# Performance work log

Hardware: AMD Instinct MI355X
Metric: run time of the kernel (lower is better)

The kernel has to match this reference:

```python
import math
import jax, jax.numpy as jnp
import numpy as np

STEP = 0.1
EPS = 1e-12


def _laplacian(src, dst, n):
    # dense symmetric-normalized Laplacian from COO edge list (symmetrized, 0/1 weights)
    A = jnp.zeros((n, n), dtype=jnp.float32).at[src, dst].set(1.0)
    A = jnp.maximum(A, A.T)
    deg = A.sum(axis=1)
    dinv = jnp.where(deg > 0, 1.0 / jnp.sqrt(jnp.maximum(deg, 1e-12)), 0.0)
    return jnp.eye(n, dtype=jnp.float32) - dinv[:, None] * A * dinv[None, :]


def _filter_bank(L, bs):
    # rational band-pass bank centered at b in arange(0,2.1,STEP):
    # D_b = sqrt(2)*a * inv((L - b I)^4 + a I),  a = (STEP/2)^4
    n = L.shape[0]
    a = (STEP / 2.0) ** 4
    I = jnp.eye(n, dtype=L.dtype)

    def one(b):
        M1 = L - b * I
        P2 = M1 @ M1
        P4 = P2 @ P2
        return math.sqrt(2.0) * a * jnp.linalg.inv(P4 + a * I)

    return jax.vmap(one)(bs)  # [F, n, n]


def _cdist_mean(e):
    # mean pairwise euclidean distance, safe sqrt on the zero diagonal
    d2 = jnp.sum((e[:, None, :] - e[None, :, :]) ** 2, axis=-1)
    d = jnp.sqrt(jnp.where(d2 > 0, d2, 1.0))
    return jnp.where(d2 > 0, d, 0.0).mean()


def setup_inputs() -> dict:
    key = jax.random.key(0)
    k1, k2, k3, k4, k5 = jax.random.split(key, 5)
    B, N, F0, R, E = 64, 128, 32, 1118, 512
    return {
        "x": jax.random.normal(k1, (B, N, F0), dtype=jnp.float32),
        "random_signal": jax.random.normal(k2, (B, N, R), dtype=jnp.float32),
        "C": jax.random.normal(k3, (21, 1), dtype=jnp.float32),
        "edge_src": jax.random.randint(k4, (B, E), 0, N),
        "edge_dst": jax.random.randint(k5, (B, E), 0, N),
        "num_classes": 4,
    }


def reference(x, random_signal, C, edge_src, edge_dst, num_classes):
    B, N, _ = x.shape
    R = random_signal.shape[-1]
    # torch.normal(0, sqrt(1/R)) random signal concatenated to features
    feats = jnp.concatenate([x, random_signal * math.sqrt(1.0 / R)], axis=-1)  # [B,N,F0+R]
    bs = jnp.arange(0.0, 2.1, STEP, dtype=jnp.float32)  # [21]
    Cn = C / jnp.maximum(jnp.linalg.norm(C, axis=0, keepdims=True), EPS)  # F.normalize(C, dim=0)

    def per_graph(src, dst, xg):
        L = _laplacian(src, dst, N)
        D = _filter_bank(L, bs)                      # [F,N,N]
        L_hat = jnp.einsum('fnm,f->nm', D, Cn[:, 0])  # D.permute(1,2,0) @ C, squeezed
        A_hat = jnp.eye(N, dtype=xg.dtype) - L_hat
        y = A_hat @ xg                                # [N, F0+R]
        z = y / jnp.maximum(jnp.linalg.norm(y, axis=1, keepdims=True), EPS)
        logits = z @ z.T                              # decode_all on normalized x
        sp = -jnp.abs(logits).sum() / (N * N)         # -||logits||_1 / n^2
        return y.mean(axis=0), sp

    emb, sp_terms = jax.vmap(per_graph)(edge_src, edge_dst, feats)  # [B,D], [B]

    # faithful repeated in-loop division: s_{i+1} = (s_i + t_i)/B  =>  sum_i t_i * B^{-(B-i)}
    i = jnp.arange(B, dtype=jnp.float32)
    w = jnp.exp(-(B - i) * jnp.log(float(B)))
    sparsity_fwd = jnp.sum(sp_terms * w)

    # labels y = arange(B) % num_classes; one positive group (class members) and
    # one negative group (non-members) per class
    idx = np.arange(B)
    hl1 = jnp.float32(0.0)
    hl2 = jnp.float32(0.0)
    for c in range(num_classes):
        pos = jnp.asarray(idx[idx % num_classes == c])
        neg = jnp.asarray(idx[idx % num_classes != c])
        beta = 1.0 / num_classes + 1e-13  # one group per class
        hl1 = hl1 + (-_cdist_mean(emb[neg])) / beta
        hl2 = hl2 + _cdist_mean(emb[pos])

    Fk = C.shape[0]
    dims = jnp.sqrt(jnp.float32(Fk))
    c_l1 = jnp.sum(jnp.abs(C), axis=0)
    c_l2 = jnp.maximum(jnp.linalg.norm(C, axis=0), EPS)
    sparsity_c = jnp.mean((dims - c_l1 / c_l2) / (dims - 1.0))

    return sparsity_c + hl2 + hl1 + sparsity_fwd
```

## Files before the change

### kernel.cpp

```cpp
#include <hip/hip_runtime.h>
#include <math.h>

#define NN 128
#define SM 129
#define TS 132
#define RS 132
#define SS 17
#define SD 130
#define EP 132

typedef double d4 __attribute__((ext_vector_type(4)));

__global__ __launch_bounds__(512, 1) void k1_lap_pow2(
    const int* __restrict__ src, const int* __restrict__ dst,
    int E, float* __restrict__ Lout, double* __restrict__ L2) {
  extern __shared__ float smf[];
  float* dinv = smf + NN * SM;
  const int g   = blockIdx.x;
  const int tid = threadIdx.x;
  const int wv = tid >> 6, ln = tid & 63;
  const int m  = ln & 15, kq = ln >> 4;

  int rIdx[4], cIdx[4];
  {
    d4 z = {0.0, 0.0, 0.0, 0.0};
    d4 pr = __builtin_amdgcn_mfma_f64_16x16x4f64((double)m, 1.0, z, 0, 0, 0);
    d4 pc = __builtin_amdgcn_mfma_f64_16x16x4f64(1.0, (double)m, z, 0, 0, 0);
#pragma unroll
    for (int r = 0; r < 4; ++r) {
      rIdx[r] = ((int)(pr[r] * 0.25 + 0.5)) & 15;
      cIdx[r] = ((int)(pc[r] * 0.25 + 0.5)) & 15;
    }
  }

  for (int e = tid; e < NN * NN; e += 512) {
    int i = e >> 7, j = e & 127;
    smf[i * SM + j] = 0.f;
  }
  __syncthreads();
  const int* s = src + (size_t)g * E;
  const int* d = dst + (size_t)g * E;
  for (int e = tid; e < E; e += 512) {
    int a = s[e], b = d[e];
    smf[a * SM + b] = 1.f;
    smf[b * SM + a] = 1.f;
  }
  __syncthreads();
  if (tid < NN) {
    float acc = 0.f;
    for (int j = 0; j < NN; ++j) acc += smf[tid * SM + j];
    dinv[tid] = (acc > 0.f) ? (float)(1.0 / sqrt((double)acc)) : 0.f;
  }
  __syncthreads();
  float* Lg = Lout + (size_t)g * NN * NN;
  for (int e = tid; e < NN * NN; e += 512) {
    int i = e >> 7, j = e & 127;
    float v = ((i == j) ? 1.f : 0.f) - dinv[i] * dinv[j] * smf[i * SM + j];
    Lg[e] = v;
    smf[i * SM + j] = v;
  }
  __syncthreads();

  d4 acc[8];
#pragma unroll
  for (int cb = 0; cb < 8; ++cb) {
    acc[cb][0] = 0.0; acc[cb][1] = 0.0; acc[cb][2] = 0.0; acc[cb][3] = 0.0;
  }
  for (int kc = 0; kc < 32; ++kc) {
    double a = (double)smf[(16 * wv + m) * SM + 4 * kc + kq];
#pragma unroll
    for (int cb = 0; cb < 8; ++cb) {
      double b = (double)smf[(4 * kc + kq) * SM + 16 * cb + m];
      acc[cb] = __builtin_amdgcn_mfma_f64_16x16x4f64(a, b, acc[cb], 0, 0, 0);
    }
  }
  double* out = L2 + (size_t)g * NN * NN;
#pragma unroll
  for (int cb = 0; cb < 8; ++cb)
#pragma unroll
    for (int r = 0; r < 4; ++r)
      out[(16 * wv + rIdx[r]) * NN + 16 * cb + cIdx[r]] = acc[cb][r];
}

__global__ __launch_bounds__(512, 1) void k1_pow34(
    const float* __restrict__ L, const double* __restrict__ L2,
    double* __restrict__ L3, double* __restrict__ L4) {
  extern __shared__ double Bs[];
  const int bid = blockIdx.x;
  const int g = bid >> 1, job = bid & 1;
  const int tid = threadIdx.x;
  const int wv = tid >> 6, ln = tid & 63;
  const int m  = ln & 15, kq = ln >> 4;

  int rIdx[4], cIdx[4];
  {
    d4 z = {0.0, 0.0, 0.0, 0.0};
    d4 pr = __builtin_amdgcn_mfma_f64_16x16x4f64((double)m, 1.0, z, 0, 0, 0);
    d4 pc = __builtin_amdgcn_mfma_f64_16x16x4f64(1.0, (double)m, z, 0, 0, 0);
#pragma unroll
    for (int r = 0; r < 4; ++r) {
      rIdx[r] = ((int)(pr[r] * 0.25 + 0.5)) & 15;
      cIdx[r] = ((int)(pc[r] * 0.25 + 0.5)) & 15;
    }
  }

  const float*  Lg  = L  + (size_t)g * NN * NN;
  const double* L2g = L2 + (size_t)g * NN * NN;
  if (job == 0) {
    for (int e = tid; e < NN * NN; e += 512) {
      int i = e >> 7, j = e & 127;
      Bs[i * SD + j] = (double)Lg[e];
    }
  } else {
    for (int e = tid; e < NN * NN; e += 512) {
      int i = e >> 7, j = e & 127;
      Bs[i * SD + j] = L2g[e];
    }
  }
  __syncthreads();

  d4 acc[8];
#pragma unroll
  for (int cb = 0; cb < 8; ++cb) {
    acc[cb][0] = 0.0; acc[cb][1] = 0.0; acc[cb][2] = 0.0; acc[cb][3] = 0.0;
  }
  for (int kc = 0; kc < 32; ++kc) {
    double a = L2g[(16 * wv + m) * NN + 4 * kc + kq];
#pragma unroll
    for (int cb = 0; cb < 8; ++cb) {
      double b = Bs[(4 * kc + kq) * SD + 16 * cb + m];
      acc[cb] = __builtin_amdgcn_mfma_f64_16x16x4f64(a, b, acc[cb], 0, 0, 0);
    }
  }
  double* out = (job == 0 ? L3 : L4) + (size_t)g * NN * NN;
#pragma unroll
  for (int cb = 0; cb < 8; ++cb)
#pragma unroll
    for (int r = 0; r < 4; ++r)
      out[(16 * wv + rIdx[r]) * NN + 16 * cb + cIdx[r]] = acc[cb][r];
}

__global__ __launch_bounds__(512, 4) void k2_filter(
    const float* __restrict__ L, const double* __restrict__ L2,
    const double* __restrict__ L3, const double* __restrict__ L4,
    const float* __restrict__ C, int NF, float* __restrict__ W) {
  extern __shared__ char smraw[];
  double* Rp  = (double*)smraw;
  double* Scd = (double*)(smraw + 16 * RS * 8);
  double* Pv  = (double*)(smraw + 16 * RS * 8 + 8 * 16 * SS * 8);

  const int bid = blockIdx.x;
  const int g = bid / NF, f = bid % NF;
  const int tid = threadIdx.x;
  const int wv = tid >> 6, ln = tid & 63;
  const int m  = ln & 15, kq = ln >> 4;
  double* S = Scd + wv * 16 * SS;

  double csum = 0.0;
  for (int q = 0; q < NF; ++q) { double c = (double)C[q]; csum += c * c; }
  double cn = sqrt(csum); if (cn < 1e-12) cn = 1e-12;
  const double a4 = 6.25e-6;
  const double coef = 1.4142135623730951 * a4 * ((double)C[f] / cn);
  const float  bf = (float)((double)f * 0.1);
  const double bb = (double)bf;
  const double c3 = -4.0 * bb;
  const double c2 = 6.0 * bb * bb;
  const double c1 = -4.0 * bb * bb * bb;
  const double c0 = bb * bb * bb * bb + a4;

  int rIdx[4], cIdx[4];
  {
    d4 z = {0.0, 0.0, 0.0, 0.0};
    d4 pr = __builtin_amdgcn_mfma_f64_16x16x4f64((double)m, 1.0, z, 0, 0, 0);
    d4 pc = __builtin_amdgcn_mfma_f64_16x16x4f64(1.0, (double)m, z, 0, 0, 0);
#pragma unroll
    for (int r = 0; r < 4; ++r) {
      rIdx[r] = ((int)(pr[r] * 0.25 + 0.5)) & 15;
      cIdx[r] = ((int)(pc[r] * 0.25 + 0.5)) & 15;
    }
  }

  const float*  Lg  = L  + (size_t)g * NN * NN;
  const double* L2g = L2 + (size_t)g * NN * NN;
  const double* L3g = L3 + (size_t)g * NN * NN;
  const double* L4g = L4 + (size_t)g * NN * NN;
  d4 T[8];
#pragma unroll
  for (int cb = 0; cb < 8; ++cb)
#pragma unroll
    for (int r = 0; r < 4; ++r) {
      int i = 16 * wv + rIdx[r], j = 16 * cb + cIdx[r];
      int idx = i * NN + j;
      double v = L4g[idx];
      v = fma(c3, L3g[idx], v);
      v = fma(c2, L2g[idx], v);
      v = fma(c1, (double)Lg[idx], v);
      if (i == j) v += c0;
      T[cb][r] = v;
    }

#pragma unroll 1
  for (int t = 0; t < 8; ++t) {
    if (wv == t) {
#pragma unroll
      for (int cb = 0; cb < 8; ++cb)
#pragma unroll
        for (int r = 0; r < 4; ++r)
          Rp[rIdx[r] * RS + 16 * cb + cIdx[r]] = T[cb][r];
    }
    __syncthreads();

    if (wv == t) {
      double sr[4];
#pragma unroll
      for (int r = 0; r < 4; ++r) sr[r] = Rp[(4 * r + kq) * RS + 16 * t + m];
#pragma unroll
      for (int k = 0; k < 16; ++k) {
        const int kr = k >> 2, kl = k & 3;
        double pv   = __shfl(sr[kr], 16 * kl + k);
        double rowv = __shfl(sr[kr], 16 * kl + m);
        double cv[4];
#pragma unroll
        for (int r = 0; r < 4; ++r) cv[r] = __shfl(sr[r], 16 * kq + k);
        double dp = 1.0 / pv;
#pragma unroll
        for (int r = 0; r < 4; ++r) {
          int i = 4 * r + kq;
          double nv;
          if (i == k)      nv = (m == k) ? dp : rowv * dp;
          else if (m == k) nv = -cv[r] * dp;
          else             nv = fma(-(cv[r] * dp), rowv, sr[r]);
          sr[r] = nv;
        }
      }
#pragma unroll
      for (int r = 0; r < 4; ++r) Pv[(4 * r + kq) * SS + m] = sr[r];
    }
    __syncthreads();

#pragma unroll
    for (int cb = 0; cb < 8; ++cb) {
      if (cb != t) continue;
      if (wv == t) {
#pragma unroll
        for (int r = 0; r < 4; ++r) T[cb][r] = Pv[rIdx[r] * SS + cIdx[r]];
      } else {
#pragma unroll
        for (int r = 0; r < 4; ++r) S[rIdx[r] * SS + cIdx[r]] = T[cb][r];
        __builtin_amdgcn_wave_barrier();
        d4 ncv = {0.0, 0.0, 0.0, 0.0};
#pragma unroll
        for (int kc = 0; kc < 4; ++kc) {
          double a = S[m * SS + 4 * kc + kq];
          double b = -Pv[(4 * kc + kq) * SS + m];
          ncv = __builtin_amdgcn_mfma_f64_16x16x4f64(a, b, ncv, 0, 0, 0);
        }
        T[cb] = ncv;
        __builtin_amdgcn_wave_barrier();
#pragma unroll
        for (int r = 0; r < 4; ++r) S[rIdx[r] * SS + cIdx[r]] = T[cb][r];
      }
    }
    __builtin_amdgcn_wave_barrier();

    const double* asrc = (wv == t) ? Pv : S;
#pragma unroll
    for (int cb = 0; cb < 8; ++cb) {
      if (cb == t) continue;
      d4 acc;
      if (wv == t) { acc[0] = 0.0; acc[1] = 0.0; acc[2] = 0.0; acc[3] = 0.0; }
      else         { acc = T[cb]; }
#pragma unroll
      for (int kc = 0; kc < 4; ++kc) {
        double a = asrc[m * SS + 4 * kc + kq];
        double b = Rp[(4 * kc + kq) * RS + 16 * cb + m];
        acc = __builtin_amdgcn_mfma_f64_16x16x4f64(a, b, acc, 0, 0, 0);
      }
      T[cb] = acc;
    }
    __syncthreads();
  }

  float* Wg = W + (size_t)g * NN * NN;
#pragma unroll
  for (int cb = 0; cb < 8; ++cb)
#pragma unroll
    for (int r = 0; r < 4; ++r)
      atomicAdd(&Wg[(16 * wv + rIdx[r]) * NN + 16 * cb + cIdx[r]],
                (float)(coef * T[cb][r]));
}

__global__ __launch_bounds__(512, 1) void k3_fused(
    const float* __restrict__ x, const float* __restrict__ rs,
    const float* __restrict__ W, float* __restrict__ G,
    float* __restrict__ emb, int F0, int R, int DTOT, int NCH,
    float rscale) {
  extern __shared__ float sm3[];
  float* ldsW = sm3;
  float* ldsX = sm3 + NN * TS;
  const int bid = blockIdx.x;
  const int g = bid / NCH;
  const int c = bid % NCH;
  const int d0 = c * 128;
  const int tid = threadIdx.x, tr = tid >> 4, tc = tid & 15;

  const float* Wg = W + (size_t)g * NN * NN;
  for (int e = tid; e < NN * NN; e += 512) {
    int k = e >> 7, i = e & 127;
    ldsW[k * TS + i] = Wg[e];
  }
  const float* xg = x + (size_t)g * NN * F0;
  const float* rg = rs + (size_t)g * NN * R;
  for (int e = tid; e < NN * NN; e += 512) {
    int k = e >> 7, dl = e & 127;
    int d = d0 + dl;
    float v = 0.f;
    if (d < DTOT) v = (d < F0) ? xg[k * F0 + d] : rg[k * R + (d - F0)] * rscale;
    ldsX[k * TS + dl] = v;
  }
  __syncthreads();

  float acc[4][8];
#pragma unroll
  for (int v = 0; v < 4; ++v)
#pragma unroll
    for (int u = 0; u < 8; ++u) acc[v][u] = 0.f;
  for (int k = 0; k < NN; ++k) {
    float4 w4 = *(const float4*)(ldsW + k * TS + 4 * tr);
    float xv[8];
#pragma unroll
    for (int u = 0; u < 8; ++u) xv[u] = ldsX[k * TS + tc + 16 * u];
    float wvv[4] = {w4.x, w4.y, w4.z, w4.w};
#pragma unroll
    for (int v = 0; v < 4; ++v)
#pragma unroll
      for (int u = 0; u < 8; ++u) acc[v][u] = fmaf(wvv[v], xv[u], acc[v][u]);
  }
#pragma unroll
  for (int v = 0; v < 4; ++v)
#pragma unroll
    for (int u = 0; u < 8; ++u)
      acc[v][u] = ldsX[(4 * tr + v) * TS + tc + 16 * u] - acc[v][u];
  __syncthreads();

#pragma unroll
  for (int v = 0; v < 4; ++v)
#pragma unroll
    for (int u = 0; u < 8; ++u)
      ldsW[(tc + 16 * u) * TS + 4 * tr + v] = acc[v][u];
#pragma unroll
  for (int u = 0; u < 8; ++u) {
    float s = 0.f;
#pragma unroll
    for (int v = 0; v < 4; ++v) s += acc[v][u];
    ldsX[tr * EP + tc + 16 * u] = s;
  }
  __syncthreads();

  float gg[4][8];
#pragma unroll
  for (int v = 0; v < 4; ++v)
#pragma unroll
    for (int u = 0; u < 8; ++u) gg[v][u] = 0.f;
  for (int dl = 0; dl < NN; ++dl) {
    float4 a4v = *(const float4*)(ldsW + dl * TS + 4 * tr);
    float bv[8];
#pragma unroll
    for (int u = 0; u < 8; ++u) bv[u] = ldsW[dl * TS + tc + 16 * u];
    float av[4] = {a4v.x, a4v.y, a4v.z, a4v.w};
#pragma unroll
    for (int v = 0; v < 4; ++v)
#pragma unroll
      for (int u = 0; u < 8; ++u) gg[v][u] = fmaf(av[v], bv[u], gg[v][u]);
  }
  float* Gg = G + (size_t)g * NN * NN;
#pragma unroll
  for (int v = 0; v < 4; ++v)
#pragma unroll
    for (int u = 0; u < 8; ++u)
      atomicAdd(&Gg[(4 * tr + v) * NN + tc + 16 * u], gg[v][u]);

  if (tid < 128) {
    int d = d0 + tid;
    if (d < DTOT) {
      float s = 0.f;
      for (int tt = 0; tt < 32; ++tt) s += ldsX[tt * EP + tid];
      emb[(size_t)g * 1152 + d] = s * (1.f / 128.f);
    }
  }
}

__global__ __launch_bounds__(256) void k45_fused(
    const float* __restrict__ G, double* __restrict__ spt,
    const float* __restrict__ emb, float* __restrict__ Dm, int DTOT) {
  __shared__ float inr[NN];
  __shared__ double red[4];
  const int bid = blockIdx.x, tid = threadIdx.x;
  if (bid < 64) {
    const int g = bid;
    const float* Gg = G + (size_t)g * NN * NN;
    if (tid < NN) {
      float n = sqrtf(fmaxf(Gg[tid * NN + tid], 0.f));
      inr[tid] = 1.f / fmaxf(n, 1e-12f);
    }
    __syncthreads();
    double s = 0.0;
    for (int e = tid; e < NN * NN; e += 256) {
      int i = e >> 7, j = e & 127;
      s += (double)(fabsf(Gg[e]) * inr[i] * inr[j]);
    }
    for (int off = 32; off; off >>= 1) s += __shfl_down(s, off);
    int wave = tid >> 6, lane = tid & 63;
    if (lane == 0) red[wave] = s;
    __syncthreads();
    if (tid == 0) spt[g] = -(red[0] + red[1] + red[2] + red[3]) / (double)(NN * NN);
  } else {
    const int i = bid - 64;
    const int wv = tid >> 6, l = tid & 63;
    float ei[18];
#pragma unroll
    for (int s = 0; s < 18; ++s) {
      int d = l + 64 * s;
      ei[s] = (d < DTOT) ? emb[(size_t)i * 1152 + d] : 0.f;
    }
    for (int jj = 0; jj < 16; ++jj) {
      int j = 4 * jj + wv;
      float acc = 0.f;
#pragma unroll
      for (int s = 0; s < 18; ++s) {
        int d = l + 64 * s;
        if (d < DTOT) {
          float df = ei[s] - emb[(size_t)j * 1152 + d];
          acc = fmaf(df, df, acc);
        }
      }
      for (int off = 32; off; off >>= 1) acc += __shfl_down(acc, off);
      if (l == 0) Dm[i * 64 + j] = (acc > 0.f) ? sqrtf(acc) : 0.f;
    }
  }
}

__global__ __launch_bounds__(64) void k5b_final(
    const float* __restrict__ Dm, const double* __restrict__ spt,
    const float* __restrict__ C, int NF,
    const int* __restrict__ ncls, float* __restrict__ out) {
  const int lane = threadIdx.x;
  const int nc = ncls[0];
  double spf = spt[lane] * exp(-((double)(64 - lane)) * log(64.0));
  for (int off = 32; off; off >>= 1) spf += __shfl_down(spf, off);

  double hl1 = 0.0, hl2 = 0.0;
  const double beta = 1.0 / (double)nc + 1e-13;
  for (int cc = 0; cc < nc; ++cc) {
    bool ip = (lane % nc) == cc;
    double ps = 0.0, ns = 0.0;
    for (int j = 0; j < 64; ++j) {
      double dv = (double)Dm[lane * 64 + j];
      bool jp = (j % nc) == cc;
      if (ip && jp) ps += dv;
      if (!ip && !jp) ns += dv;
    }
    for (int off = 32; off; off >>= 1) {
      ps += __shfl_down(ps, off);
      ns += __shfl_down(ns, off);
    }
    int npos = 0;
    for (int q = 0; q < 64; ++q) if (q % nc == cc) npos++;
    int nneg = 64 - npos;
    hl2 += ps / ((double)npos * (double)npos);
    hl1 += -(ns / ((double)nneg * (double)nneg)) / beta;
  }
  if (lane == 0) {
    double l1 = 0.0, l2 = 0.0;
    for (int q = 0; q < NF; ++q) { double cv = (double)C[q]; l1 += fabs(cv); l2 += cv * cv; }
    l2 = sqrt(l2); if (l2 < 1e-12) l2 = 1e-12;
    double dims = sqrt((double)NF);
    double sc = (dims - l1 / l2) / (dims - 1.0);
    out[0] = (float)(sc + hl2 + hl1 + spf);
  }
}

extern "C" void kernel_launch(void* const* d_in, const int* in_sizes, int n_in,
                              void* d_out, int out_size, void* d_ws, size_t ws_size,
                              hipStream_t stream) {
  (void)n_in; (void)out_size; (void)ws_size;
  const float* x    = (const float*)d_in[0];
  const float* rs   = (const float*)d_in[1];
  const float* C    = (const float*)d_in[2];
  const int*   esrc = (const int*)d_in[3];
  const int*   edst = (const int*)d_in[4];
  const int*   ncls = (const int*)d_in[5];
  float* out = (float*)d_out;

  const int F0   = in_sizes[0] / (64 * 128);
  const int R    = in_sizes[1] / (64 * 128);
  const int NF   = in_sizes[2];
  const int E    = in_sizes[3] / 64;
  const int DTOT = F0 + R;
  const int NCH  = (DTOT + 127) / 128;
  const float rscale = (float)(1.0 / sqrt((double)R));

  char* ws = (char*)d_ws;
  size_t off = 0;
  float*  L    = (float*)(ws + off);  off += (size_t)64 * NN * NN * 4;
  float*  W    = (float*)(ws + off);  off += (size_t)64 * NN * NN * 4;
  float*  G    = (float*)(ws + off);  off += (size_t)64 * NN * NN * 4;
  double* L2d  = (double*)(ws + off); off += (size_t)64 * NN * NN * 8;
  double* L3d  = (double*)(ws + off); off += (size_t)64 * NN * NN * 8;
  double* L4d  = (double*)(ws + off); off += (size_t)64 * NN * NN * 8;
  float*  emb  = (float*)(ws + off);  off += (size_t)64 * 1152 * 4;
  double* spt  = (double*)(ws + off); off += (size_t)64 * 8;
  float*  Dm   = (float*)(ws + off);  off += (size_t)64 * 64 * 4;

  hipMemsetAsync(W, 0, (size_t)2 * 64 * NN * NN * 4, stream);

  const int lds1 = (NN * SM + NN) * 4;
  const int ldsp = NN * SD * 8;
  const int lds2 = 16 * RS * 8 + 8 * 16 * SS * 8 + 16 * SS * 8;
  const int lds3 = NN * TS * 4 * 2;
  hipFuncSetAttribute((const void*)k1_lap_pow2, hipFuncAttributeMaxDynamicSharedMemorySize, lds1);
  hipFuncSetAttribute((const void*)k1_pow34,    hipFuncAttributeMaxDynamicSharedMemorySize, ldsp);
  hipFuncSetAttribute((const void*)k2_filter,   hipFuncAttributeMaxDynamicSharedMemorySize, lds2);
  hipFuncSetAttribute((const void*)k3_fused,    hipFuncAttributeMaxDynamicSharedMemorySize, lds3);

  k1_lap_pow2<<<64, 512, lds1, stream>>>(esrc, edst, E, L, L2d);
  k1_pow34<<<128, 512, ldsp, stream>>>(L, L2d, L3d, L4d);
  k2_filter<<<64 * NF, 512, lds2, stream>>>(L, L2d, L3d, L4d, C, NF, W);
  k3_fused<<<64 * NCH, 512, lds3, stream>>>(x, rs, W, G, emb, F0, R, DTOT, NCH, rscale);
  k45_fused<<<128, 256, 0, stream>>>(G, spt, emb, Dm, DTOT);
  k5b_final<<<1, 64, 0, stream>>>(Dm, spt, C, NF, ncls, out);
}
```

Baseline: 641.2 us.

## Split Laplacian build from squaring and spread matrix powers over more blocks

Moves the Laplacian construction into its own small kernel and gives L^2 a separate kernel that splits each graph's product across 4 blocks. L^3/L^4 are also split by row half, so 256 blocks replace 128. With only 64 or 128 blocks on a GPU with 256 CUs, the FP64 MFMA work left most compute units idle; the finer split aims to fill the device. In exchange it adds a kernel launch, redundant LDS staging of the full B matrix in every block, and an extra round trip of L through global memory.

```diff
diff --git a/kernel.cpp b/kernel.cpp
--- a/kernel.cpp
+++ b/kernel.cpp
@@ -11,15 +11,51 @@
 
 typedef double d4 __attribute__((ext_vector_type(4)));
 
-__global__ __launch_bounds__(512, 1) void k1_lap_pow2(
+__global__ __launch_bounds__(256) void k1_lap(
     const int* __restrict__ src, const int* __restrict__ dst,
-    int E, float* __restrict__ Lout, double* __restrict__ L2) {
-  extern __shared__ float smf[];
-  float* dinv = smf + NN * SM;
+    int E, float* __restrict__ Lout) {
+  extern __shared__ float sm1[];
+  float* A    = sm1;
+  float* dinv = sm1 + NN * SM;
   const int g   = blockIdx.x;
+  const int tid = threadIdx.x;
+
+  for (int e = tid; e < NN * NN; e += 256) {
+    int i = e >> 7, j = e & 127;
+    A[i * SM + j] = 0.f;
+  }
+  __syncthreads();
+  const int* s = src + (size_t)g * E;
+  const int* d = dst + (size_t)g * E;
+  for (int e = tid; e < E; e += 256) {
+    int a = s[e], b = d[e];
+    A[a * SM + b] = 1.f;
+    A[b * SM + a] = 1.f;
+  }
+  __syncthreads();
+  if (tid < NN) {
+    float acc = 0.f;
+    for (int j = 0; j < NN; ++j) acc += A[tid * SM + j];
+    dinv[tid] = (acc > 0.f) ? (float)(1.0 / sqrt((double)acc)) : 0.f;
+  }
+  __syncthreads();
+  float* Lg = Lout + (size_t)g * NN * NN;
+  for (int e = tid; e < NN * NN; e += 256) {
+    int i = e >> 7, j = e & 127;
+    Lg[e] = ((i == j) ? 1.f : 0.f) - dinv[i] * dinv[j] * A[i * SM + j];
+  }
+}
+
+__global__ __launch_bounds__(512, 1) void kpow2(
+    const float* __restrict__ L, double* __restrict__ L2) {
+  extern __shared__ double Bs[];
+  const int bid = blockIdx.x;
+  const int g = bid >> 2, q = bid & 3;
   const int tid = threadIdx.x;
   const int wv = tid >> 6, ln = tid & 63;
   const int m  = ln & 15, kq = ln >> 4;
+  const int rb = 32 * q + 16 * (wv & 1);
+  const int cb0 = 2 * (wv >> 1);
 
   int rIdx[4], cIdx[4];
   {
@@ -33,64 +69,45 @@
     }
   }
 
+  const float* Lg = L + (size_t)g * NN * NN;
   for (int e = tid; e < NN * NN; e += 512) {
     int i = e >> 7, j = e & 127;
-    smf[i * SM + j] = 0.f;
-  }
-  __syncthreads();
-  const int* s = src + (size_t)g * E;
-  const int* d = dst + (size_t)g * E;
-  for (int e = tid; e < E; e += 512) {
-    int a = s[e], b = d[e];
-    smf[a * SM + b] = 1.f;
-    smf[b * SM + a] = 1.f;
-  }
-  __syncthreads();
-  if (tid < NN) {
-    float acc = 0.f;
-    for (int j = 0; j < NN; ++j) acc += smf[tid * SM + j];
-    dinv[tid] = (acc > 0.f) ? (float)(1.0 / sqrt((double)acc)) : 0.f;
-  }
-  __syncthreads();
-  float* Lg = Lout + (size_t)g * NN * NN;
-  for (int e = tid; e < NN * NN; e += 512) {
-    int i = e >> 7, j = e & 127;
-    float v = ((i == j) ? 1.f : 0.f) - dinv[i] * dinv[j] * smf[i * SM + j];
-    Lg[e] = v;
-    smf[i * SM + j] = v;
-  }
-  __syncthreads();
-
-  d4 acc[8];
-#pragma unroll
-  for (int cb = 0; cb < 8; ++cb) {
-    acc[cb][0] = 0.0; acc[cb][1] = 0.0; acc[cb][2] = 0.0; acc[cb][3] = 0.0;
+    Bs[i * SD + j] = (double)Lg[e];
+  }
+  __syncthreads();
+
+  d4 acc[2];
+#pragma unroll
+  for (int c = 0; c < 2; ++c) {
+    acc[c][0] = 0.0; acc[c][1] = 0.0; acc[c][2] = 0.0; acc[c][3] = 0.0;
   }
   for (int kc = 0; kc < 32; ++kc) {
-    double a = (double)smf[(16 * wv + m) * SM + 4 * kc + kq];
-#pragma unroll
-    for (int cb = 0; cb < 8; ++cb) {
-      double b = (double)smf[(4 * kc + kq) * SM + 16 * cb + m];
-      acc[cb] = __builtin_amdgcn_mfma_f64_16x16x4f64(a, b, acc[cb], 0, 0, 0);
+    double a = Bs[(rb + m) * SD + 4 * kc + kq];
+#pragma unroll
+    for (int c = 0; c < 2; ++c) {
+      double b = Bs[(4 * kc + kq) * SD + 16 * (cb0 + c) + m];
+      acc[c] = __builtin_amdgcn_mfma_f64_16x16x4f64(a, b, acc[c], 0, 0, 0);
     }
   }
   double* out = L2 + (size_t)g * NN * NN;
 #pragma unroll
-  for (int cb = 0; cb < 8; ++cb)
+  for (int c = 0; c < 2; ++c)
 #pragma unroll
     for (int r = 0; r < 4; ++r)
-      out[(16 * wv + rIdx[r]) * NN + 16 * cb + cIdx[r]] = acc[cb][r];
-}
-
-__global__ __launch_bounds__(512, 1) void k1_pow34(
+      out[(rb + rIdx[r]) * NN + 16 * (cb0 + c) + cIdx[r]] = acc[c][r];
+}
+
+__global__ __launch_bounds__(512, 1) void kpow34(
     const float* __restrict__ L, const double* __restrict__ L2,
     double* __restrict__ L3, double* __restrict__ L4) {
   extern __shared__ double Bs[];
   const int bid = blockIdx.x;
-  const int g = bid >> 1, job = bid & 1;
+  const int g = bid >> 2, h = (bid >> 1) & 1, job = bid & 1;
   const int tid = threadIdx.x;
   const int wv = tid >> 6, ln = tid & 63;
   const int m  = ln & 15, kq = ln >> 4;
+  const int rb = 64 * h + 16 * (wv & 3);
+  const int cb0 = 4 * (wv >> 2);
 
   int rIdx[4], cIdx[4];
   {
@@ -119,25 +136,25 @@
   }
   __syncthreads();
 
-  d4 acc[8];
-#pragma unroll
-  for (int cb = 0; cb < 8; ++cb) {
-    acc[cb][0] = 0.0; acc[cb][1] = 0.0; acc[cb][2] = 0.0; acc[cb][3] = 0.0;
+  d4 acc[4];
+#pragma unroll
+  for (int c = 0; c < 4; ++c) {
+    acc[c][0] = 0.0; acc[c][1] = 0.0; acc[c][2] = 0.0; acc[c][3] = 0.0;
   }
   for (int kc = 0; kc < 32; ++kc) {
-    double a = L2g[(16 * wv + m) * NN + 4 * kc + kq];
-#pragma unroll
-    for (int cb = 0; cb < 8; ++cb) {
-      double b = Bs[(4 * kc + kq) * SD + 16 * cb + m];
-      acc[cb] = __builtin_amdgcn_mfma_f64_16x16x4f64(a, b, acc[cb], 0, 0, 0);
+    double a = L2g[(rb + m) * NN + 4 * kc + kq];
+#pragma unroll
+    for (int c = 0; c < 4; ++c) {
+      double b = Bs[(4 * kc + kq) * SD + 16 * (cb0 + c) + m];
+      acc[c] = __builtin_amdgcn_mfma_f64_16x16x4f64(a, b, acc[c], 0, 0, 0);
     }
   }
   double* out = (job == 0 ? L3 : L4) + (size_t)g * NN * NN;
 #pragma unroll
-  for (int cb = 0; cb < 8; ++cb)
+  for (int c = 0; c < 4; ++c)
 #pragma unroll
     for (int r = 0; r < 4; ++r)
-      out[(16 * wv + rIdx[r]) * NN + 16 * cb + cIdx[r]] = acc[cb][r];
+      out[(rb + rIdx[r]) * NN + 16 * (cb0 + c) + cIdx[r]] = acc[c][r];
 }
 
 __global__ __launch_bounds__(512, 4) void k2_filter(
@@ -518,13 +535,15 @@
   const int ldsp = NN * SD * 8;
   const int lds2 = 16 * RS * 8 + 8 * 16 * SS * 8 + 16 * SS * 8;
   const int lds3 = NN * TS * 4 * 2;
-  hipFuncSetAttribute((const void*)k1_lap_pow2, hipFuncAttributeMaxDynamicSharedMemorySize, lds1);
-  hipFuncSetAttribute((const void*)k1_pow34,    hipFuncAttributeMaxDynamicSharedMemorySize, ldsp);
-  hipFuncSetAttribute((const void*)k2_filter,   hipFuncAttributeMaxDynamicSharedMemorySize, lds2);
-  hipFuncSetAttribute((const void*)k3_fused,    hipFuncAttributeMaxDynamicSharedMemorySize, lds3);
-
-  k1_lap_pow2<<<64, 512, lds1, stream>>>(esrc, edst, E, L, L2d);
-  k1_pow34<<<128, 512, ldsp, stream>>>(L, L2d, L3d, L4d);
+  hipFuncSetAttribute((const void*)k1_lap,    hipFuncAttributeMaxDynamicSharedMemorySize, lds1);
+  hipFuncSetAttribute((const void*)kpow2,     hipFuncAttributeMaxDynamicSharedMemorySize, ldsp);
+  hipFuncSetAttribute((const void*)kpow34,    hipFuncAttributeMaxDynamicSharedMemorySize, ldsp);
+  hipFuncSetAttribute((const void*)k2_filter, hipFuncAttributeMaxDynamicSharedMemorySize, lds2);
+  hipFuncSetAttribute((const void*)k3_fused,  hipFuncAttributeMaxDynamicSharedMemorySize, lds3);
+
+  k1_lap<<<64, 256, lds1, stream>>>(esrc, edst, E, L);
+  kpow2<<<256, 512, ldsp, stream>>>(L, L2d);
+  kpow34<<<256, 512, ldsp, stream>>>(L, L2d, L3d, L4d);
   k2_filter<<<64 * NF, 512, lds2, stream>>>(L, L2d, L3d, L4d, C, NF, W);
   k3_fused<<<64 * NCH, 512, lds3, stream>>>(x, rs, W, G, emb, F0, R, DTOT, NCH, rscale);
   k45_fused<<<128, 256, 0, stream>>>(G, spt, emb, Dm, DTOT);
```

After: 638.5 us. No clear change (-0.4%).
